# Kernel tuning notes

Measured on AMD Instinct MI355X. Metric: run time of the kernel, lower is better.

## Reference

```python
import jax, jax.numpy as jnp
import numpy as np

N = 8192
D = 256
E = 262144


def setup_inputs() -> dict:
    key = jax.random.key(0)
    kx, ke = jax.random.split(key)
    x = jax.random.normal(kx, (N, D), dtype=jnp.float32)
    edge_index = jax.random.randint(ke, (2, E), 0, N, dtype=jnp.int64)
    return {"x": x, "edge_index": edge_index}


def reference(x, edge_index):
    n, d = x.shape
    xs = x / (d ** 0.25)
    # per-edge similarity: equivalent to einsum('md,nd->mn')[src, dst] without O(n^2 d)
    src, dst = edge_index[0], edge_index[1]
    vals = jnp.einsum('ed,ed->e', xs[src], xs[dst])
    neg = jnp.finfo(jnp.float32).min
    sim = jnp.full((n, n), neg, dtype=x.dtype)
    sim = sim.at[src, dst].set(vals)
    # logaritmic=False branch: plain double softmax, averaged
    scores0 = jax.nn.softmax(sim, axis=1)                # row softmax
    scores1 = jax.nn.softmax(sim, axis=0)                # col softmax (== softmax(sim.T, -1).T)
    scores = (scores0 + scores1) * 0.5
    return scores, sim
```

## Files before the change

### kernel.cpp

```cpp
#include <hip/hip_runtime.h>
#include <float.h>
#include <math.h>

constexpr int Nn = 8192;
constexpr unsigned BG = 0xFF7F0000u;

typedef unsigned u32x4 __attribute__((ext_vector_type(4)));

__device__ __forceinline__ float clamp01(float f) {
    return fminf(fmaxf(f, 0.0f), 1.0f);
}

__device__ __forceinline__ void load_edge(const unsigned* ew, unsigned F, int E, int e,
                                          int& s, int& d) {
    s = (int)(ew[e << F] & (Nn - 1));
    d = (int)(ew[(E << F) + (e << F)] & (Nn - 1));
}

__global__ void k1_fill(u32x4* __restrict__ sim4, const unsigned* __restrict__ ew,
                        unsigned* __restrict__ flag, float* __restrict__ rowsum,
                        float* __restrict__ colsum) {
    int tid = blockIdx.x * 256 + threadIdx.x;
    u32x4 bg = {BG, BG, BG, BG};
    sim4[tid] = bg;
    if (tid < Nn) {
        rowsum[tid] = 0.0f;
        colsum[tid] = 0.0f;
    }
    if (blockIdx.x == 0) {
        __shared__ unsigned acc;
        if (threadIdx.x == 0) acc = 0u;
        __syncthreads();
        atomicOr(&acc, ew[2 * threadIdx.x + 1]);
        __syncthreads();
        if (threadIdx.x == 0) flag[0] = (acc == 0u) ? 1u : 0u;
    }
}

__global__ void k2_edges(const float* __restrict__ x, const unsigned* __restrict__ ew,
                         const unsigned* __restrict__ flag, unsigned* __restrict__ sim_u,
                         float* __restrict__ vals,
                         float* __restrict__ rowsum, float* __restrict__ colsum, int E) {
    int e = (blockIdx.x << 2) + (threadIdx.x >> 6);
    if (e >= E) return;
    int lane = threadIdx.x & 63;
    unsigned F = flag[0];
    int s, d;
    load_edge(ew, F, E, e, s, d);
    const float4* xa = (const float4*)x + (((size_t)s) << 6) + lane;
    const float4* xb = (const float4*)x + (((size_t)d) << 6) + lane;
    float4 a = *xa;
    float4 b = *xb;
    float v = a.x * b.x + a.y * b.y + a.z * b.z + a.w * b.w;
    #pragma unroll
    for (int off = 32; off; off >>= 1) v += __shfl_xor(v, off);
    v *= 0.0625f;
    if (lane == 0) {
        vals[e] = v;
        unsigned cell = (unsigned)s * (unsigned)Nn + (unsigned)d;
        unsigned old = atomicExch(&sim_u[cell], __float_as_uint(v));
        if (old == BG) {
            float ev = expf(v);
            atomicAdd(&rowsum[s], ev);
            atomicAdd(&colsum[d], ev);
        }
    }
}

__global__ void k3_stats(const float* __restrict__ rowsum, const float* __restrict__ colsum,
                         float* __restrict__ r_row, float* __restrict__ c_col,
                         float* __restrict__ hr, float* __restrict__ hc) {
    int i = blockIdx.x * 256 + threadIdx.x;
    float sr = rowsum[i];
    float bg = (sr == 0.0f) ? 1.0f : 0.0f;
    float ss = sr + (float)Nn * bg;
    r_row[i] = bg / ss;
    hr[i] = 0.5f / ss;
    sr = colsum[i];
    bg = (sr == 0.0f) ? 1.0f : 0.0f;
    ss = sr + (float)Nn * bg;
    c_col[i] = bg / ss;
    hc[i] = 0.5f / ss;
}

__global__ void k4_fix(float* __restrict__ scores, const float* __restrict__ r_row,
                       const float* __restrict__ c_col) {
    int b = blockIdx.x;
    if (b < Nn) {
        float ri = r_row[b];
        if (ri == 0.0f) return;
        for (int j = threadIdx.x; j < Nn; j += 256)
            scores[(size_t)b * Nn + j] = clamp01(0.5f * (ri + c_col[j]));
    } else {
        int j = b - Nn;
        float cj = c_col[j];
        if (cj == 0.0f) return;
        for (int i = threadIdx.x; i < Nn; i += 256)
            scores[(size_t)i * Nn + j] = clamp01(0.5f * (r_row[i] + cj));
    }
}

__global__ void k5_scatter(const unsigned* __restrict__ ew, const unsigned* __restrict__ flag,
                           const float* __restrict__ vals,
                           const float* __restrict__ hr, const float* __restrict__ hc,
                           float* __restrict__ scores, int E) {
    int e = blockIdx.x * 256 + threadIdx.x;
    if (e >= E) return;
    unsigned F = flag[0];
    int s, d;
    load_edge(ew, F, E, e, s, d);
    float sc = clamp01(expf(vals[e]) * (hr[s] + hc[d]));
    scores[(size_t)s * Nn + d] = sc;
}

extern "C" void kernel_launch(void* const* d_in, const int* in_sizes, int n_in,
                              void* d_out, int out_size, void* d_ws, size_t ws_size,
                              hipStream_t stream) {
    const float* x = (const float*)d_in[0];
    const unsigned* ew = (const unsigned*)d_in[1];
    const int E = in_sizes[1] / 2;

    float* scores = (float*)d_out;
    float* sim = scores + (size_t)Nn * (size_t)Nn;

    char* w = (char*)d_ws;
    unsigned* flag = (unsigned*)w;  w += 16;
    float* vals = (float*)w;        w += (size_t)E * 4;
    float* rowsum = (float*)w;      w += (size_t)Nn * 4;
    float* colsum = (float*)w;      w += (size_t)Nn * 4;
    float* r_row = (float*)w;       w += (size_t)Nn * 4;
    float* c_col = (float*)w;       w += (size_t)Nn * 4;
    float* hr = (float*)w;          w += (size_t)Nn * 4;
    float* hc = (float*)w;          w += (size_t)Nn * 4;

    constexpr int FILL_BLOCKS = (Nn / 4) * Nn / 256;
    k1_fill<<<FILL_BLOCKS, 256, 0, stream>>>((u32x4*)sim, ew, flag, rowsum, colsum);
    k2_edges<<<(E + 3) / 4, 256, 0, stream>>>(x, ew, flag, (unsigned*)sim, vals,
                                              rowsum, colsum, E);
    k3_stats<<<Nn / 256, 256, 0, stream>>>(rowsum, colsum, r_row, c_col, hr, hc);
    k4_fix<<<2 * Nn, 256, 0, stream>>>(scores, r_row, c_col);
    k5_scatter<<<(E + 255) / 256, 256, 0, stream>>>(ew, flag, vals, hr, hc, scores, E);
}
```

Baseline: 604.9 us.

## Fuse stats, background fix and edge scatter into one kernel; widen edge and fill work

Removes the separate stats and scatter kernels by recomputing the per-row and per-column normalisers inline from rowsum and colsum inside a single output kernel. That kernel handles both the edge scatter blocks and the empty row and column fix blocks. Their writes cannot conflict, because only rows and columns without edges are rewritten. The edge kernel now assigns 16 lanes per edge, with four float4 loads each and a shorter shuffle reduction, in place of one 64-lane wave per edge. The fill kernel writes two vectors per thread. The aim is fewer launches, fewer intermediate arrays and better per-thread work granularity, at the cost of some redundant reciprocal math.

```diff
diff --git a/kernel.cpp b/kernel.cpp
--- a/kernel.cpp
+++ b/kernel.cpp
@@ -17,12 +17,20 @@
     d = (int)(ew[(E << F) + (e << F)] & (Nn - 1));
 }
 
+__device__ __forceinline__ float stat_ss(float sr) {
+    return sr + (sr == 0.0f ? (float)Nn : 0.0f);
+}
+__device__ __forceinline__ float stat_bgp(float sr) {
+    return (sr == 0.0f) ? (1.0f / (float)Nn) : 0.0f;
+}
+
 __global__ void k1_fill(u32x4* __restrict__ sim4, const unsigned* __restrict__ ew,
                         unsigned* __restrict__ flag, float* __restrict__ rowsum,
                         float* __restrict__ colsum) {
     int tid = blockIdx.x * 256 + threadIdx.x;
     u32x4 bg = {BG, BG, BG, BG};
-    sim4[tid] = bg;
+    sim4[2 * tid] = bg;
+    sim4[2 * tid + 1] = bg;
     if (tid < Nn) {
         rowsum[tid] = 0.0f;
         colsum[tid] = 0.0f;
@@ -41,21 +49,28 @@
                          const unsigned* __restrict__ flag, unsigned* __restrict__ sim_u,
                          float* __restrict__ vals,
                          float* __restrict__ rowsum, float* __restrict__ colsum, int E) {
-    int e = (blockIdx.x << 2) + (threadIdx.x >> 6);
+    int lane = threadIdx.x & 63;
+    int wid = threadIdx.x >> 6;
+    int g = lane >> 4;
+    int t = lane & 15;
+    int e = (blockIdx.x * 4 + wid) * 4 + g;
     if (e >= E) return;
-    int lane = threadIdx.x & 63;
     unsigned F = flag[0];
     int s, d;
     load_edge(ew, F, E, e, s, d);
-    const float4* xa = (const float4*)x + (((size_t)s) << 6) + lane;
-    const float4* xb = (const float4*)x + (((size_t)d) << 6) + lane;
-    float4 a = *xa;
-    float4 b = *xb;
-    float v = a.x * b.x + a.y * b.y + a.z * b.z + a.w * b.w;
+    const float4* xa = (const float4*)x + (((size_t)s) << 6);
+    const float4* xb = (const float4*)x + (((size_t)d) << 6);
+    float v = 0.0f;
     #pragma unroll
-    for (int off = 32; off; off >>= 1) v += __shfl_xor(v, off);
+    for (int i = 0; i < 4; ++i) {
+        float4 a = xa[t + 16 * i];
+        float4 b = xb[t + 16 * i];
+        v += a.x * b.x + a.y * b.y + a.z * b.z + a.w * b.w;
+    }
+    #pragma unroll
+    for (int off = 8; off; off >>= 1) v += __shfl_xor(v, off);
     v *= 0.0625f;
-    if (lane == 0) {
+    if (t == 0) {
         vals[e] = v;
         unsigned cell = (unsigned)s * (unsigned)Nn + (unsigned)d;
         unsigned old = atomicExch(&sim_u[cell], __float_as_uint(v));
@@ -67,50 +82,36 @@
     }
 }
 
-__global__ void k3_stats(const float* __restrict__ rowsum, const float* __restrict__ colsum,
-                         float* __restrict__ r_row, float* __restrict__ c_col,
-                         float* __restrict__ hr, float* __restrict__ hc) {
-    int i = blockIdx.x * 256 + threadIdx.x;
-    float sr = rowsum[i];
-    float bg = (sr == 0.0f) ? 1.0f : 0.0f;
-    float ss = sr + (float)Nn * bg;
-    r_row[i] = bg / ss;
-    hr[i] = 0.5f / ss;
-    sr = colsum[i];
-    bg = (sr == 0.0f) ? 1.0f : 0.0f;
-    ss = sr + (float)Nn * bg;
-    c_col[i] = bg / ss;
-    hc[i] = 0.5f / ss;
-}
-
-__global__ void k4_fix(float* __restrict__ scores, const float* __restrict__ r_row,
-                       const float* __restrict__ c_col) {
+__global__ void k3_out(const unsigned* __restrict__ ew, const unsigned* __restrict__ flag,
+                       const float* __restrict__ vals,
+                       const float* __restrict__ rowsum, const float* __restrict__ colsum,
+                       float* __restrict__ scores, int E, int EB) {
     int b = blockIdx.x;
-    if (b < Nn) {
-        float ri = r_row[b];
+    if (b < EB) {
+        int e = b * 256 + threadIdx.x;
+        if (e >= E) return;
+        unsigned F = flag[0];
+        int s, d;
+        load_edge(ew, F, E, e, s, d);
+        float hr = 0.5f / stat_ss(rowsum[s]);
+        float hc = 0.5f / stat_ss(colsum[d]);
+        float sc = clamp01(expf(vals[e]) * (hr + hc));
+        scores[(size_t)s * Nn + d] = sc;
+        return;
+    }
+    int r = b - EB;
+    if (r < Nn) {
+        float ri = stat_bgp(rowsum[r]);
         if (ri == 0.0f) return;
         for (int j = threadIdx.x; j < Nn; j += 256)
-            scores[(size_t)b * Nn + j] = clamp01(0.5f * (ri + c_col[j]));
+            scores[(size_t)r * Nn + j] = clamp01(0.5f * (ri + stat_bgp(colsum[j])));
     } else {
-        int j = b - Nn;
-        float cj = c_col[j];
+        int j = r - Nn;
+        float cj = stat_bgp(colsum[j]);
         if (cj == 0.0f) return;
         for (int i = threadIdx.x; i < Nn; i += 256)
-            scores[(size_t)i * Nn + j] = clamp01(0.5f * (r_row[i] + cj));
+            scores[(size_t)i * Nn + j] = clamp01(0.5f * (stat_bgp(rowsum[i]) + cj));
     }
-}
-
-__global__ void k5_scatter(const unsigned* __restrict__ ew, const unsigned* __restrict__ flag,
-                           const float* __restrict__ vals,
-                           const float* __restrict__ hr, const float* __restrict__ hc,
-                           float* __restrict__ scores, int E) {
-    int e = blockIdx.x * 256 + threadIdx.x;
-    if (e >= E) return;
-    unsigned F = flag[0];
-    int s, d;
-    load_edge(ew, F, E, e, s, d);
-    float sc = clamp01(expf(vals[e]) * (hr[s] + hc[d]));
-    scores[(size_t)s * Nn + d] = sc;
 }
 
 extern "C" void kernel_launch(void* const* d_in, const int* in_sizes, int n_in,
@@ -128,16 +129,10 @@
     float* vals = (float*)w;        w += (size_t)E * 4;
     float* rowsum = (float*)w;      w += (size_t)Nn * 4;
     float* colsum = (float*)w;      w += (size_t)Nn * 4;
-    float* r_row = (float*)w;       w += (size_t)Nn * 4;
-    float* c_col = (float*)w;       w += (size_t)Nn * 4;
-    float* hr = (float*)w;          w += (size_t)Nn * 4;
-    float* hc = (float*)w;          w += (size_t)Nn * 4;
 
-    constexpr int FILL_BLOCKS = (Nn / 4) * Nn / 256;
-    k1_fill<<<FILL_BLOCKS, 256, 0, stream>>>((u32x4*)sim, ew, flag, rowsum, colsum);
-    k2_edges<<<(E + 3) / 4, 256, 0, stream>>>(x, ew, flag, (unsigned*)sim, vals,
-                                              rowsum, colsum, E);
-    k3_stats<<<Nn / 256, 256, 0, stream>>>(rowsum, colsum, r_row, c_col, hr, hc);
-    k4_fix<<<2 * Nn, 256, 0, stream>>>(scores, r_row, c_col);
-    k5_scatter<<<(E + 255) / 256, 256, 0, stream>>>(ew, flag, vals, hr, hc, scores, E);
+    const int EB = (E + 255) / 256;
+    k1_fill<<<(Nn / 8) * Nn / 256, 256, 0, stream>>>((u32x4*)sim, ew, flag, rowsum, colsum);
+    k2_edges<<<(E + 15) / 16, 256, 0, stream>>>(x, ew, flag, (unsigned*)sim, vals,
+                                                rowsum, colsum, E);
+    k3_out<<<EB + 2 * Nn, 256, 0, stream>>>(ew, flag, vals, rowsum, colsum, scores, E, EB);
 }
```

Measured after the change: 570.5 us. -5.7%, faster.
